# Kernel optimization log

Measured on AMD Instinct MI355X. Metric: run time of the kernel, lower is better.

The kernel has to match this reference:

```python
import jax, jax.numpy as jnp
import numpy as np
import math

B, S, E, H = 2, 2048, 1024, 16
HD = E // H          # head_dim = 64
HX = 64              # helix_dim
P = HX // 2          # helix pairs = 32

def setup_inputs() -> dict:
    key = jax.random.key(0)
    ks = jax.random.split(key, 12)
    sc = 0.02
    return {
        "x":    jax.random.normal(ks[0], (B, S, E), dtype=jnp.float32),
        "Wq":   jax.random.normal(ks[1], (E, E), dtype=jnp.float32) * sc,
        "bq":   jnp.zeros((E,), dtype=jnp.float32),
        "Wk":   jax.random.normal(ks[2], (E, E), dtype=jnp.float32) * sc,
        "bk":   jnp.zeros((E,), dtype=jnp.float32),
        "Wv":   jax.random.normal(ks[3], (E, E), dtype=jnp.float32) * sc,
        "bv":   jnp.zeros((E,), dtype=jnp.float32),
        "Wo":   jax.random.normal(ks[4], (E, E), dtype=jnp.float32) * sc,
        "bo":   jnp.zeros((E,), dtype=jnp.float32),
        "Whel": jax.random.normal(ks[5], (H, HX, HD), dtype=jnp.float32) * sc,
        "bhel": jnp.zeros((H, HX), dtype=jnp.float32),
    }

def _l2norm(x, eps=1e-12):
    # torch F.normalize(p=2, dim=-1): x / max(||x||, eps)
    n = jnp.sqrt(jnp.sum(x * x, axis=-1, keepdims=True))
    return x / jnp.maximum(n, eps)

def _scramble(t):
    # faithful to torch: (B,S,2) -> transpose(1,2) -> reshape(B,S,2),
    # vectorized over (H,P): t is (B,H,P,S,2)
    b, h, p, s, _ = t.shape
    return jnp.swapaxes(t, -1, -2).reshape(b, h, p, s, 2)

def reference(x, Wq, bq, Wk, bk, Wv, bv, Wo, bo, Whel, bhel):
    b, s, e = x.shape
    h, hx, hd = Whel.shape
    p = hx // 2
    q = x @ Wq.T + bq
    k = x @ Wk.T + bk
    v = x @ Wv.T + bv
    qh = q.reshape(b, s, h, hd)
    kh = k.reshape(b, s, h, hd)
    # per-head helical projections: (B,S,H,HX)
    q_hel = jnp.einsum('bshd,hed->bshe', qh, Whel) + bhel
    k_hel = jnp.einsum('bshd,hed->bshe', kh, Whel) + bhel
    # split into 2D coords, normalize each pair: (B,H,P,S,2)
    qn = _l2norm(q_hel.reshape(b, s, h, p, 2)).transpose(0, 2, 3, 1, 4)
    kn = _l2norm(k_hel.reshape(b, s, h, p, 2)).transpose(0, 2, 3, 1, 4)
    qn = _scramble(qn)
    kn = _scramble(kn)
    # helical similarity averaged over pairs: (B,H,S,S)
    helical = jnp.einsum('bhpsc,bhptc->bhst', qn, kn) / p
    # standard scaled dot-product scores
    dot = jnp.einsum('bshd,bthd->bhst', qh, kh) / math.sqrt(hd)
    alpha = 0.5
    attn = jax.nn.softmax(alpha * dot + (1.0 - alpha) * helical, axis=-1)
    vh = v.reshape(b, s, h, hd)
    out = jnp.einsum('bhst,bthd->bshd', attn, vh).reshape(b, s, e)
    return out @ Wo.T + bo
```

## Files before the change

kernel.cpp:

```cpp
#include <hip/hip_runtime.h>
#include <hip/hip_bf16.h>


typedef unsigned short u16;
typedef unsigned int u32;
typedef __attribute__((ext_vector_type(8))) __bf16 bf16x8;
typedef __attribute__((ext_vector_type(4))) float f32x4;
typedef __attribute__((ext_vector_type(16))) float f32x16;

union BFrag { u32 u[4]; bf16x8 b; };

__device__ __forceinline__ u16 f2b(float f) {
  u32 u = __float_as_uint(f);
  u32 r = (u + 0x7fffu + ((u >> 16) & 1u)) >> 16;
  return (u16)r;
}
__device__ __forceinline__ float b2f(u16 h) {
  return __uint_as_float(((u32)h) << 16);
}

__device__ __forceinline__ f32x4 mfma16(bf16x8 a, bf16x8 b, f32x4 c) {
  return __builtin_amdgcn_mfma_f32_16x16x32_bf16(a, b, c, 0, 0, 0);
}
__device__ __forceinline__ f32x16 mfma32(bf16x8 a, bf16x8 b, f32x16 c) {
  return __builtin_amdgcn_mfma_f32_32x32x16_bf16(a, b, c, 0, 0, 0);
}

__device__ __forceinline__ void gld16(void* lds, const void* g) {
  __builtin_amdgcn_global_load_lds(
      (const __attribute__((address_space(1))) unsigned int*)g,
      (__attribute__((address_space(3))) unsigned int*)lds, 16, 0, 0);
}

#define LOG2E 1.4426950408889634f

__global__ __launch_bounds__(256) void cast_kernel(
    const float* __restrict__ x,  const float* __restrict__ wq,
    const float* __restrict__ wk, const float* __restrict__ wv,
    const float* __restrict__ wo, const float* __restrict__ whel,
    u16* __restrict__ xb, u16* __restrict__ wb, u16* __restrict__ wob,
    u16* __restrict__ whb) {
  long long q = (long long)blockIdx.x * 256 + threadIdx.x;
  const float* s; u16* d; long long base;
  if (q < 1048576)      { s = x;    d = xb;            base = 0; }
  else if (q < 1310720) { s = wq;   d = wb;            base = 1048576; }
  else if (q < 1572864) { s = wk;   d = wb + 1048576;  base = 1310720; }
  else if (q < 1835008) { s = wv;   d = wb + 2097152;  base = 1572864; }
  else if (q < 2097152) { s = wo;   d = wob;           base = 1835008; }
  else                  { s = whel; d = whb;           base = 2097152; }
  long long e = (q - base) * 4;
  float4 v = *(const float4*)(s + e);
  ushort4 o;
  o.x = f2b(v.x); o.y = f2b(v.y); o.z = f2b(v.z); o.w = f2b(v.w);
  *(ushort4*)(d + e) = o;
}

__global__ __launch_bounds__(256, 3) void qkv_gemm(
    const u16* __restrict__ xb, const u16* __restrict__ wb,
    const float* __restrict__ bq, const float* __restrict__ bk,
    const float* __restrict__ bv,
    u16* __restrict__ Qcat, u16* __restrict__ Kcat, u16* __restrict__ vt) {
  __shared__ u16 Al[2][128][32];
  __shared__ u16 Bl[2][128][32];
  __shared__ u16 T[64][136];
  const int nt = blockIdx.x, mt = blockIdx.y;
  const int which = nt >> 3;
  const int n0 = (nt & 7) << 7;
  const int m0 = mt << 7;
  const int tid = threadIdx.x;
  const int wave = tid >> 6, lane = tid & 63;
  const int g = lane >> 4, c15 = lane & 15;
  const int wm = wave & 1, wn = wave >> 1;
  const u16* Wp = wb + (long long)which * (1024 * 1024) + n0 * 1024;
  const u16* Ap = xb + m0 * 1024;
  const int srow = (wave * 64 + lane) >> 2;
  const int scol = (lane & 3) << 3;

  f32x4 acc[4][4];
#pragma unroll
  for (int i = 0; i < 4; i++)
#pragma unroll
    for (int j = 0; j < 4; j++) acc[i][j] = f32x4{0.f, 0.f, 0.f, 0.f};

  gld16(&Al[0][srow][scol],      Ap + srow * 1024 + scol);
  gld16(&Al[0][64 + srow][scol], Ap + (64 + srow) * 1024 + scol);
  gld16(&Bl[0][srow][scol],      Wp + srow * 1024 + scol);
  gld16(&Bl[0][64 + srow][scol], Wp + (64 + srow) * 1024 + scol);

  for (int k0 = 0; k0 < 1024; k0 += 32) {
    const int c = (k0 >> 5) & 1;
    __syncthreads();
    if (k0 + 32 < 1024) {
      const int kn = k0 + 32;
      gld16(&Al[c ^ 1][srow][scol],      Ap + srow * 1024 + kn + scol);
      gld16(&Al[c ^ 1][64 + srow][scol], Ap + (64 + srow) * 1024 + kn + scol);
      gld16(&Bl[c ^ 1][srow][scol],      Wp + srow * 1024 + kn + scol);
      gld16(&Bl[c ^ 1][64 + srow][scol], Wp + (64 + srow) * 1024 + kn + scol);
    }
    bf16x8 a[4], b[4];
#pragma unroll
    for (int i = 0; i < 4; i++)
      a[i] = *(const bf16x8*)&Al[c][wm * 64 + i * 16 + c15][g * 8];
#pragma unroll
    for (int j = 0; j < 4; j++)
      b[j] = *(const bf16x8*)&Bl[c][wn * 64 + j * 16 + c15][g * 8];
#pragma unroll
    for (int i = 0; i < 4; i++)
#pragma unroll
      for (int j = 0; j < 4; j++) acc[i][j] = mfma16(a[i], b[j], acc[i][j]);
  }

  if (which == 2) {
#pragma unroll
    for (int half = 0; half < 2; ++half) {
      __syncthreads();
      if (wn == half) {
#pragma unroll
        for (int i = 0; i < 4; i++)
#pragma unroll
          for (int j = 0; j < 4; j++)
#pragma unroll
            for (int r = 0; r < 4; r++) {
              int nloc = j * 16 + c15;
              int mloc = wm * 64 + i * 16 + g * 4 + r;
              float v = acc[i][j][r] + bv[n0 + half * 64 + nloc];
              T[nloc][mloc] = f2b(v);
            }
      }
      __syncthreads();
#pragma unroll
      for (int it = 0; it < 4; ++it) {
        int idx = it * 256 + tid;
        int row = idx >> 4;
        int cm = (idx & 15) * 8;
        int col = n0 + half * 64 + row;
        int hh = col >> 6, dd = col & 63;
        int m = m0 + cm;
        int bb2 = m >> 11, s = m & 2047;
        *(uint4*)&vt[(((bb2 * 16 + hh) * 64) + dd) * 2048 + s] =
            *(const uint4*)&T[row][cm];
      }
    }
    return;
  }

  const float* bias = (which == 0) ? bq : bk;
#pragma unroll
  for (int i = 0; i < 4; i++)
#pragma unroll
    for (int j = 0; j < 4; j++)
#pragma unroll
      for (int r = 0; r < 4; r++) {
        int row = m0 + wm * 64 + i * 16 + g * 4 + r;
        int col = n0 + wn * 64 + j * 16 + c15;
        float v = acc[i][j][r] + bias[col];
        int bb = row >> 11, s = row & 2047;
        int hh = col >> 6, d = col & 63;
        if (which == 0) {
          Qcat[(((bb * 16 + hh) * 2048) + s) * 128 + d] =
              f2b(v * (0.0625f * LOG2E));
        } else {
          Kcat[(((bb * 16 + hh) * 2048) + s) * 128 + d] = f2b(v);
        }
      }
}

__global__ __launch_bounds__(256, 2) void helical_kernel(
    u16* __restrict__ Qcat, u16* __restrict__ Kcat,
    const u16* __restrict__ whb, const float* __restrict__ bhel) {
  __shared__ u16 A[2][2][64][32];
  __shared__ u16 Wl[2][64][32];
  const int sb = blockIdx.x, bh = blockIdx.y;
  const int h = bh & 15;
  const int s0 = sb << 6;
  const int tid = threadIdx.x;
  const int wave = tid >> 6, lane = tid & 63;
  const int g = lane >> 4, c15 = lane & 15;
  u16* Qb = Qcat + (long long)bh * (2048 * 128);
  u16* Kb = Kcat + (long long)bh * (2048 * 128);

#pragma unroll
  for (int it = 0; it < 2; ++it) {
    int cidx = it * 256 + tid;
    int e = cidx >> 3, ds = (cidx & 7) << 3;
    uint4 vv = *(const uint4*)(whb + h * 4096 + e * 64 + ds);
    *(uint4*)&Wl[ds >> 5][e][ds & 31] = vv;
  }
#pragma unroll
  for (int it = 0; it < 4; ++it) {
    int cidx = it * 256 + tid;
    int which = cidx >> 9;
    int r = (cidx >> 3) & 63;
    int ds = (cidx & 7) << 3;
    const u16* src = (which ? Kb : Qb) + (s0 + r) * 128 + ds;
    uint4 vv = *(const uint4*)src;
    if (which == 0) {
      u16 tmp[8];
      *(uint4*)tmp = vv;
#pragma unroll
      for (int q = 0; q < 8; ++q)
        tmp[q] = f2b(b2f(tmp[q]) * (16.0f / LOG2E));
      vv = *(uint4*)tmp;
    }
    *(uint4*)&A[which][ds >> 5][r][ds & 31] = vv;
  }
  __syncthreads();

  const int which = wave >> 1, hf = wave & 1;
  f32x4 acc[2][4];
#pragma unroll
  for (int i = 0; i < 2; i++)
#pragma unroll
    for (int j = 0; j < 4; j++) acc[i][j] = f32x4{0.f, 0.f, 0.f, 0.f};
#pragma unroll
  for (int kq = 0; kq < 2; ++kq) {
    bf16x8 a0 = *(const bf16x8*)&A[which][kq][hf * 32 + c15][g * 8];
    bf16x8 a1 = *(const bf16x8*)&A[which][kq][hf * 32 + 16 + c15][g * 8];
#pragma unroll
    for (int j = 0; j < 4; ++j) {
      bf16x8 bb = *(const bf16x8*)&Wl[kq][j * 16 + c15][g * 8];
      acc[0][j] = mfma16(a0, bb, acc[0][j]);
      acc[1][j] = mfma16(a1, bb, acc[1][j]);
    }
  }
  u16* Dst = which ? Kb : Qb;
  const float oscale = which ? 0.125f : (0.125f * LOG2E);
#pragma unroll
  for (int i = 0; i < 2; ++i)
#pragma unroll
    for (int j = 0; j < 4; ++j)
#pragma unroll
      for (int r = 0; r < 4; ++r) {
        int s_loc = hf * 32 + i * 16 + g * 4 + r;
        int e = j * 16 + c15;
        float v = acc[i][j][r] + bhel[h * 64 + e];
        float pp = __shfl_xor(v, 1);
        float nn = sqrtf(v * v + pp * pp);
        float o = v / fmaxf(nn, 1e-12f) * oscale;
        int s = s0 + s_loc;
        int u = s >> 1, c2 = s & 1;
        int row_out = ((e & 1) ? 1024 : 0) + u;
        int col_out = 64 + (e & ~1) + c2;
        Dst[row_out * 128 + col_out] = f2b(o);
      }
}

__global__ __launch_bounds__(256, 2) void attn_kernel(
    const u16* __restrict__ Qcat, const u16* __restrict__ Kcat,
    const u16* __restrict__ vt, u16* __restrict__ AO) {
  __shared__ u16 Kl[2][64][128];
  __shared__ u16 Vl[2][64][64];
  __shared__ float denl[2][128];
  const int qt = blockIdx.x, bh = blockIdx.y;
  const int bb = bh >> 4, h = bh & 15;
  const int q0 = qt << 7;
  const int tid = threadIdx.x;
  const int w = tid >> 6, lane = tid & 63;
  const int wq2 = w & 1, wt = w >> 1;
  const int l31 = lane & 31, l5 = lane >> 5;
  const u16* Qb = Qcat + (long long)bh * (2048 * 128);
  const u16* Kb = Kcat + (long long)bh * (2048 * 128);
  const u16* Vb = vt + (long long)bh * (64 * 2048);

  bf16x8 qf[2][8];
#pragma unroll
  for (int qh = 0; qh < 2; ++qh) {
    const u16* qrow = Qb + (q0 + 64 * wq2 + 32 * qh + l31) * 128 + l5 * 8;
#pragma unroll
    for (int ks = 0; ks < 8; ++ks)
      qf[qh][ks] = *(const bf16x8*)(qrow + ks * 16);
  }

  int krowR[4], ksrcR[4];
#pragma unroll
  for (int rk = 0; rk < 4; ++rk) {
    int id = rk * 256 + tid;
    int row = id >> 4, kp = id & 15;
    krowR[rk] = row;
    ksrcR[rk] = (kp & 8) | ((kp & 7) ^ (row & 7));
  }
  int vdR[2], vsrcR[2];
#pragma unroll
  for (int rv = 0; rv < 2; ++rv) {
    int id = rv * 256 + tid;
    int d = id >> 3;
    vdR[rv] = d;
    vsrcR[rv] = (id & 7) ^ (d & 7);
  }

#pragma unroll
  for (int rk = 0; rk < 4; ++rk)
    gld16(((u16*)Kl[0]) + (rk * 256 + tid) * 8,
          Kb + krowR[rk] * 128 + ksrcR[rk] * 8);
#pragma unroll
  for (int rv = 0; rv < 2; ++rv)
    gld16(((u16*)Vl[0]) + (rv * 256 + tid) * 8,
          Vb + vdR[rv] * 2048 + vsrcR[rv] * 8);

  f32x16 accO[2][2];
#pragma unroll
  for (int a = 0; a < 2; ++a)
#pragma unroll
    for (int b = 0; b < 2; ++b)
#pragma unroll
      for (int i = 0; i < 16; ++i) accO[a][b][i] = 0.f;
  float den[2] = {0.f, 0.f};

  const int krow = 32 * wt + l31;
  const int kr7 = krow & 7;

  for (int t = 0; t < 32; ++t) {
    const int cur = t & 1;
    __syncthreads();
    if (t + 1 < 32) {
      const int t1 = (t + 1) << 6;
      u16* Kd = (u16*)Kl[cur ^ 1];
      u16* Vd = (u16*)Vl[cur ^ 1];
#pragma unroll
      for (int rk = 0; rk < 4; ++rk)
        gld16(Kd + (rk * 256 + tid) * 8,
              Kb + (t1 + krowR[rk]) * 128 + ksrcR[rk] * 8);
#pragma unroll
      for (int rv = 0; rv < 2; ++rv)
        gld16(Vd + (rv * 256 + tid) * 8,
              Vb + vdR[rv] * 2048 + t1 + vsrcR[rv] * 8);
    }

    f32x16 accS0, accS1;
#pragma unroll
    for (int i = 0; i < 16; ++i) { accS0[i] = 0.f; accS1[i] = 0.f; }
#pragma unroll
    for (int ks = 0; ks < 8; ++ks) {
      int lc = 2 * ks + l5;
      int p = (lc & 8) | ((lc & 7) ^ kr7);
      bf16x8 ak = *(const bf16x8*)&Kl[cur][krow][p * 8];
      accS0 = mfma32(ak, qf[0][ks], accS0);
      accS1 = mfma32(ak, qf[1][ks], accS1);
    }

    BFrag PA[2][2];
#pragma unroll
    for (int qh = 0; qh < 2; ++qh) {
      const f32x16& s = qh ? accS1 : accS0;
      u32 D0[2], D1[2], D2[2], D3[2];
#pragma unroll
      for (int rr = 0; rr < 4; ++rr) {
        float p0 = __builtin_amdgcn_exp2f(s[4 * rr + 0]);
        float p1 = __builtin_amdgcn_exp2f(s[4 * rr + 1]);
        float p2 = __builtin_amdgcn_exp2f(s[4 * rr + 2]);
        float p3 = __builtin_amdgcn_exp2f(s[4 * rr + 3]);
        den[qh] += (p0 + p1) + (p2 + p3);
        u32 lo =
            (__float_as_uint(p0) >> 16) | (__float_as_uint(p1) & 0xffff0000u);
        u32 hi =
            (__float_as_uint(p2) >> 16) | (__float_as_uint(p3) & 0xffff0000u);
        if (rr == 0) { D0[0] = lo; D0[1] = hi; }
        else if (rr == 1) { D1[0] = lo; D1[1] = hi; }
        else if (rr == 2) { D2[0] = lo; D2[1] = hi; }
        else { D3[0] = lo; D3[1] = hi; }
      }
      u32 e00 = __shfl_xor((int)D0[0], 32), e01 = __shfl_xor((int)D0[1], 32);
      u32 e10 = __shfl_xor((int)D1[0], 32), e11 = __shfl_xor((int)D1[1], 32);
      u32 e20 = __shfl_xor((int)D2[0], 32), e21 = __shfl_xor((int)D2[1], 32);
      u32 e30 = __shfl_xor((int)D3[0], 32), e31 = __shfl_xor((int)D3[1], 32);
      PA[qh][0].u[0] = l5 ? e10 : D0[0];
      PA[qh][0].u[1] = l5 ? e11 : D0[1];
      PA[qh][0].u[2] = l5 ? D1[0] : e00;
      PA[qh][0].u[3] = l5 ? D1[1] : e01;
      PA[qh][1].u[0] = l5 ? e30 : D2[0];
      PA[qh][1].u[1] = l5 ? e31 : D2[1];
      PA[qh][1].u[2] = l5 ? D3[0] : e20;
      PA[qh][1].u[3] = l5 ? D3[1] : e21;
    }

#pragma unroll
    for (int dq = 0; dq < 2; ++dq) {
      int d = 32 * dq + l31;
      int d7 = d & 7;
#pragma unroll
      for (int ks = 0; ks < 2; ++ks) {
        int lc = 4 * wt + 2 * ks + l5;
        bf16x8 bvf = *(const bf16x8*)&Vl[cur][d][((lc ^ d7) & 7) * 8];
        accO[0][dq] = mfma32(PA[0][ks].b, bvf, accO[0][dq]);
        accO[1][dq] = mfma32(PA[1][ks].b, bvf, accO[1][dq]);
      }
    }
  }

  den[0] += __shfl_xor(den[0], 32);
  den[1] += __shfl_xor(den[1], 32);
  if (l5 == 0) {
    denl[wt][64 * wq2 + l31] = den[0];
    denl[wt][64 * wq2 + 32 + l31] = den[1];
  }
  __syncthreads();

  float* S = (float*)Kl;
  if (wt == 1) {
#pragma unroll
    for (int qh = 0; qh < 2; ++qh)
#pragma unroll
      for (int dq = 0; dq < 2; ++dq)
#pragma unroll
        for (int r = 0; r < 16; ++r) {
          int qr = (r & 3) + 8 * (r >> 2) + 4 * l5;
          S[(64 * wq2 + 32 * qh + qr) * 64 + 32 * dq + l31] = accO[qh][dq][r];
        }
  }
  __syncthreads();
  if (wt == 0) {
#pragma unroll
    for (int qh = 0; qh < 2; ++qh)
#pragma unroll
      for (int r = 0; r < 16; ++r) {
        int qr = (r & 3) + 8 * (r >> 2) + 4 * l5;
        int ql = 64 * wq2 + 32 * qh + qr;
        float inv = 1.0f / (denl[0][ql] + denl[1][ql]);
        long long base = ((long long)(bb * 2048 + q0 + ql) * 1024) + h * 64;
#pragma unroll
        for (int dq = 0; dq < 2; ++dq) {
          float o = (accO[qh][dq][r] + S[ql * 64 + 32 * dq + l31]) * inv;
          AO[base + 32 * dq + l31] = f2b(o);
        }
      }
  }
}

__global__ __launch_bounds__(256, 2) void out_gemm(
    const u16* __restrict__ AO, const u16* __restrict__ wob,
    const float* __restrict__ bo, float* __restrict__ out) {
  __shared__ u16 Al[2][128][32];
  __shared__ u16 Bl[2][128][32];
  const int n0 = blockIdx.x << 7;
  const int m0 = blockIdx.y << 7;
  const int tid = threadIdx.x;
  const int wave = tid >> 6, lane = tid & 63;
  const int g = lane >> 4, c15 = lane & 15;
  const int wm = wave & 1, wn = wave >> 1;
  const u16* Wp = wob + n0 * 1024;
  const u16* Ap = AO + m0 * 1024;
  const int srow = (wave * 64 + lane) >> 2;
  const int scol = (lane & 3) << 3;

  f32x4 acc[4][4];
#pragma unroll
  for (int i = 0; i < 4; i++)
#pragma unroll
    for (int j = 0; j < 4; j++) acc[i][j] = f32x4{0.f, 0.f, 0.f, 0.f};

  gld16(&Al[0][srow][scol],      Ap + srow * 1024 + scol);
  gld16(&Al[0][64 + srow][scol], Ap + (64 + srow) * 1024 + scol);
  gld16(&Bl[0][srow][scol],      Wp + srow * 1024 + scol);
  gld16(&Bl[0][64 + srow][scol], Wp + (64 + srow) * 1024 + scol);

  for (int k0 = 0; k0 < 1024; k0 += 32) {
    const int c = (k0 >> 5) & 1;
    __syncthreads();
    if (k0 + 32 < 1024) {
      const int kn = k0 + 32;
      gld16(&Al[c ^ 1][srow][scol],      Ap + srow * 1024 + kn + scol);
      gld16(&Al[c ^ 1][64 + srow][scol], Ap + (64 + srow) * 1024 + kn + scol);
      gld16(&Bl[c ^ 1][srow][scol],      Wp + srow * 1024 + kn + scol);
      gld16(&Bl[c ^ 1][64 + srow][scol], Wp + (64 + srow) * 1024 + kn + scol);
    }
    bf16x8 a[4], b[4];
#pragma unroll
    for (int i = 0; i < 4; i++)
      a[i] = *(const bf16x8*)&Al[c][wm * 64 + i * 16 + c15][g * 8];
#pragma unroll
    for (int j = 0; j < 4; j++)
      b[j] = *(const bf16x8*)&Bl[c][wn * 64 + j * 16 + c15][g * 8];
#pragma unroll
    for (int i = 0; i < 4; i++)
#pragma unroll
      for (int j = 0; j < 4; j++) acc[i][j] = mfma16(a[i], b[j], acc[i][j]);
  }
#pragma unroll
  for (int i = 0; i < 4; i++)
#pragma unroll
    for (int j = 0; j < 4; j++)
#pragma unroll
      for (int r = 0; r < 4; r++) {
        int row = m0 + wm * 64 + i * 16 + g * 4 + r;
        int col = n0 + wn * 64 + j * 16 + c15;
        out[row * 1024 + col] = acc[i][j][r] + bo[col];
      }
}

extern "C" void kernel_launch(void* const* d_in, const int* in_sizes, int n_in,
                              void* d_out, int out_size, void* d_ws,
                              size_t ws_size, hipStream_t stream) {
  const float* x    = (const float*)d_in[0];
  const float* Wq   = (const float*)d_in[1];
  const float* bq   = (const float*)d_in[2];
  const float* Wk   = (const float*)d_in[3];
  const float* bk   = (const float*)d_in[4];
  const float* Wv   = (const float*)d_in[5];
  const float* bv   = (const float*)d_in[6];
  const float* Wo   = (const float*)d_in[7];
  const float* bo   = (const float*)d_in[8];
  const float* Whel = (const float*)d_in[9];
  const float* bhel = (const float*)d_in[10];
  float* out = (float*)d_out;

  char* ws = (char*)d_ws;
  u16* xb   = (u16*)(ws + 0);
  u16* wb   = (u16*)(ws + 8388608);
  u16* wob  = (u16*)(ws + 14680064);
  u16* whb  = (u16*)(ws + 16777216);
  u16* Qcat = (u16*)(ws + 16908288);
  u16* Kcat = (u16*)(ws + 33685504);
  u16* vt   = (u16*)(ws + 50462720);
  u16* AO   = (u16*)(ws + 58851328);

  cast_kernel<<<dim3(8256), dim3(256), 0, stream>>>(x, Wq, Wk, Wv, Wo, Whel,
                                                    xb, wb, wob, whb);
  qkv_gemm<<<dim3(24, 32), dim3(256), 0, stream>>>(xb, wb, bq, bk, bv, Qcat,
                                                   Kcat, vt);
  helical_kernel<<<dim3(32, 32), dim3(256), 0, stream>>>(Qcat, Kcat, whb,
                                                         bhel);
  attn_kernel<<<dim3(16, 32), dim3(256), 0, stream>>>(Qcat, Kcat, vt, AO);
  out_gemm<<<dim3(8, 32), dim3(256), 0, stream>>>(AO, wob, bo, out);
}
```

Measured before the change: 232.1 us.

## Load attention K/V fragments directly into registers, drop LDS and cross-wave reduction

The attention kernel now runs 2 waves per block, each owning 64 query rows and iterating over all keys. K and V fragments are loaded from global memory straight into registers with a two-stage software double buffer, replacing the LDS staging and per-iteration barriers. The end-of-kernel LDS reduction across key-split waves is replaced by an in-register normalization using a shuffled denominator and a fast reciprocal. This removes synchronization and LDS traffic, but lowers occupancy and loses K/V sharing across waves, adding more global/L2 reads and high register pressure.

Result: slower. 271.6 us (+17.0%).

```diff
diff --git a/kernel.cpp b/kernel.cpp
--- a/kernel.cpp
+++ b/kernel.cpp
@@ -245,19 +245,15 @@
       }
 }
 
-__global__ __launch_bounds__(256, 2) void attn_kernel(
+__global__ __launch_bounds__(128, 1) void attn_kernel(
     const u16* __restrict__ Qcat, const u16* __restrict__ Kcat,
     const u16* __restrict__ vt, u16* __restrict__ AO) {
-  __shared__ u16 Kl[2][64][128];
-  __shared__ u16 Vl[2][64][64];
-  __shared__ float denl[2][128];
-  const int qt = blockIdx.x, bh = blockIdx.y;
+  const int qg = blockIdx.x, bh = blockIdx.y;
   const int bb = bh >> 4, h = bh & 15;
-  const int q0 = qt << 7;
   const int tid = threadIdx.x;
   const int w = tid >> 6, lane = tid & 63;
-  const int wq2 = w & 1, wt = w >> 1;
   const int l31 = lane & 31, l5 = lane >> 5;
+  const int qw = qg * 128 + w * 64;
   const u16* Qb = Qcat + (long long)bh * (2048 * 128);
   const u16* Kb = Kcat + (long long)bh * (2048 * 128);
   const u16* Vb = vt + (long long)bh * (64 * 2048);
@@ -265,37 +261,14 @@
   bf16x8 qf[2][8];
 #pragma unroll
   for (int qh = 0; qh < 2; ++qh) {
-    const u16* qrow = Qb + (q0 + 64 * wq2 + 32 * qh + l31) * 128 + l5 * 8;
+    const u16* qrow = Qb + (qw + 32 * qh + l31) * 128 + l5 * 8;
 #pragma unroll
     for (int ks = 0; ks < 8; ++ks)
       qf[qh][ks] = *(const bf16x8*)(qrow + ks * 16);
   }
 
-  int krowR[4], ksrcR[4];
-#pragma unroll
-  for (int rk = 0; rk < 4; ++rk) {
-    int id = rk * 256 + tid;
-    int row = id >> 4, kp = id & 15;
-    krowR[rk] = row;
-    ksrcR[rk] = (kp & 8) | ((kp & 7) ^ (row & 7));
-  }
-  int vdR[2], vsrcR[2];
-#pragma unroll
-  for (int rv = 0; rv < 2; ++rv) {
-    int id = rv * 256 + tid;
-    int d = id >> 3;
-    vdR[rv] = d;
-    vsrcR[rv] = (id & 7) ^ (d & 7);
-  }
-
-#pragma unroll
-  for (int rk = 0; rk < 4; ++rk)
-    gld16(((u16*)Kl[0]) + (rk * 256 + tid) * 8,
-          Kb + krowR[rk] * 128 + ksrcR[rk] * 8);
-#pragma unroll
-  for (int rv = 0; rv < 2; ++rv)
-    gld16(((u16*)Vl[0]) + (rv * 256 + tid) * 8,
-          Vb + vdR[rv] * 2048 + vsrcR[rv] * 8);
+  const u16* kbase = Kb + l31 * 128 + l5 * 8;
+  const u16* vbase = Vb + l31 * 2048 + l5 * 8;
 
   f32x16 accO[2][2];
 #pragma unroll
@@ -306,124 +279,107 @@
       for (int i = 0; i < 16; ++i) accO[a][b][i] = 0.f;
   float den[2] = {0.f, 0.f};
 
-  const int krow = 32 * wt + l31;
-  const int kr7 = krow & 7;
-
-  for (int t = 0; t < 32; ++t) {
-    const int cur = t & 1;
-    __syncthreads();
-    if (t + 1 < 32) {
-      const int t1 = (t + 1) << 6;
-      u16* Kd = (u16*)Kl[cur ^ 1];
-      u16* Vd = (u16*)Vl[cur ^ 1];
-#pragma unroll
-      for (int rk = 0; rk < 4; ++rk)
-        gld16(Kd + (rk * 256 + tid) * 8,
-              Kb + (t1 + krowR[rk]) * 128 + ksrcR[rk] * 8);
-#pragma unroll
-      for (int rv = 0; rv < 2; ++rv)
-        gld16(Vd + (rv * 256 + tid) * 8,
-              Vb + vdR[rv] * 2048 + t1 + vsrcR[rv] * 8);
-    }
-
-    f32x16 accS0, accS1;
-#pragma unroll
-    for (int i = 0; i < 16; ++i) { accS0[i] = 0.f; accS1[i] = 0.f; }
-#pragma unroll
-    for (int ks = 0; ks < 8; ++ks) {
-      int lc = 2 * ks + l5;
-      int p = (lc & 8) | ((lc & 7) ^ kr7);
-      bf16x8 ak = *(const bf16x8*)&Kl[cur][krow][p * 8];
-      accS0 = mfma32(ak, qf[0][ks], accS0);
-      accS1 = mfma32(ak, qf[1][ks], accS1);
-    }
-
-    BFrag PA[2][2];
-#pragma unroll
-    for (int qh = 0; qh < 2; ++qh) {
-      const f32x16& s = qh ? accS1 : accS0;
-      u32 D0[2], D1[2], D2[2], D3[2];
-#pragma unroll
-      for (int rr = 0; rr < 4; ++rr) {
-        float p0 = __builtin_amdgcn_exp2f(s[4 * rr + 0]);
-        float p1 = __builtin_amdgcn_exp2f(s[4 * rr + 1]);
-        float p2 = __builtin_amdgcn_exp2f(s[4 * rr + 2]);
-        float p3 = __builtin_amdgcn_exp2f(s[4 * rr + 3]);
-        den[qh] += (p0 + p1) + (p2 + p3);
-        u32 lo =
-            (__float_as_uint(p0) >> 16) | (__float_as_uint(p1) & 0xffff0000u);
-        u32 hi =
-            (__float_as_uint(p2) >> 16) | (__float_as_uint(p3) & 0xffff0000u);
-        if (rr == 0) { D0[0] = lo; D0[1] = hi; }
-        else if (rr == 1) { D1[0] = lo; D1[1] = hi; }
-        else if (rr == 2) { D2[0] = lo; D2[1] = hi; }
-        else { D3[0] = lo; D3[1] = hi; }
-      }
-      u32 e00 = __shfl_xor((int)D0[0], 32), e01 = __shfl_xor((int)D0[1], 32);
-      u32 e10 = __shfl_xor((int)D1[0], 32), e11 = __shfl_xor((int)D1[1], 32);
-      u32 e20 = __shfl_xor((int)D2[0], 32), e21 = __shfl_xor((int)D2[1], 32);
-      u32 e30 = __shfl_xor((int)D3[0], 32), e31 = __shfl_xor((int)D3[1], 32);
-      PA[qh][0].u[0] = l5 ? e10 : D0[0];
-      PA[qh][0].u[1] = l5 ? e11 : D0[1];
-      PA[qh][0].u[2] = l5 ? D1[0] : e00;
-      PA[qh][0].u[3] = l5 ? D1[1] : e01;
-      PA[qh][1].u[0] = l5 ? e30 : D2[0];
-      PA[qh][1].u[1] = l5 ? e31 : D2[1];
-      PA[qh][1].u[2] = l5 ? D3[0] : e20;
-      PA[qh][1].u[3] = l5 ? D3[1] : e21;
-    }
-
-#pragma unroll
-    for (int dq = 0; dq < 2; ++dq) {
-      int d = 32 * dq + l31;
-      int d7 = d & 7;
-#pragma unroll
-      for (int ks = 0; ks < 2; ++ks) {
-        int lc = 4 * wt + 2 * ks + l5;
-        bf16x8 bvf = *(const bf16x8*)&Vl[cur][d][((lc ^ d7) & 7) * 8];
-        accO[0][dq] = mfma32(PA[0][ks].b, bvf, accO[0][dq]);
-        accO[1][dq] = mfma32(PA[1][ks].b, bvf, accO[1][dq]);
-      }
-    }
+  auto ldt = [&](int t, bf16x8 (&kf)[2][8], bf16x8 (&vf)[2][4]) {
+    const u16* kt = kbase + t * 8192;
+#pragma unroll
+    for (int sl = 0; sl < 2; ++sl)
+#pragma unroll
+      for (int ks = 0; ks < 8; ++ks)
+        kf[sl][ks] = *(const bf16x8*)(kt + sl * 4096 + ks * 16);
+    const u16* vtp = vbase + t * 64;
+#pragma unroll
+    for (int dq = 0; dq < 2; ++dq)
+#pragma unroll
+      for (int c = 0; c < 4; ++c)
+        vf[dq][c] = *(const bf16x8*)(vtp + dq * 65536 + c * 16);
+  };
+
+  auto step = [&](bf16x8 (&kf)[2][8], bf16x8 (&vf)[2][4]) {
+    f32x16 aS[2][2];
+#pragma unroll
+    for (int sl = 0; sl < 2; ++sl)
+#pragma unroll
+      for (int qh = 0; qh < 2; ++qh)
+#pragma unroll
+        for (int i = 0; i < 16; ++i) aS[sl][qh][i] = 0.f;
+#pragma unroll
+    for (int sl = 0; sl < 2; ++sl)
+#pragma unroll
+      for (int ks = 0; ks < 8; ++ks) {
+        bf16x8 ak = kf[sl][ks];
+        aS[sl][0] = mfma32(ak, qf[0][ks], aS[sl][0]);
+        aS[sl][1] = mfma32(ak, qf[1][ks], aS[sl][1]);
+      }
+#pragma unroll
+    for (int sl = 0; sl < 2; ++sl) {
+      BFrag PA[2][2];
+#pragma unroll
+      for (int qh = 0; qh < 2; ++qh) {
+        u32 D0[2], D1[2], D2[2], D3[2];
+#pragma unroll
+        for (int rr = 0; rr < 4; ++rr) {
+          float p0 = __builtin_amdgcn_exp2f(aS[sl][qh][4 * rr + 0]);
+          float p1 = __builtin_amdgcn_exp2f(aS[sl][qh][4 * rr + 1]);
+          float p2 = __builtin_amdgcn_exp2f(aS[sl][qh][4 * rr + 2]);
+          float p3 = __builtin_amdgcn_exp2f(aS[sl][qh][4 * rr + 3]);
+          den[qh] += (p0 + p1) + (p2 + p3);
+          u32 lo = (__float_as_uint(p0) >> 16) |
+                   (__float_as_uint(p1) & 0xffff0000u);
+          u32 hi = (__float_as_uint(p2) >> 16) |
+                   (__float_as_uint(p3) & 0xffff0000u);
+          if (rr == 0) { D0[0] = lo; D0[1] = hi; }
+          else if (rr == 1) { D1[0] = lo; D1[1] = hi; }
+          else if (rr == 2) { D2[0] = lo; D2[1] = hi; }
+          else { D3[0] = lo; D3[1] = hi; }
+        }
+        u32 e00 = __shfl_xor((int)D0[0], 32), e01 = __shfl_xor((int)D0[1], 32);
+        u32 e10 = __shfl_xor((int)D1[0], 32), e11 = __shfl_xor((int)D1[1], 32);
+        u32 e20 = __shfl_xor((int)D2[0], 32), e21 = __shfl_xor((int)D2[1], 32);
+        u32 e30 = __shfl_xor((int)D3[0], 32), e31 = __shfl_xor((int)D3[1], 32);
+        PA[qh][0].u[0] = l5 ? e10 : D0[0];
+        PA[qh][0].u[1] = l5 ? e11 : D0[1];
+        PA[qh][0].u[2] = l5 ? D1[0] : e00;
+        PA[qh][0].u[3] = l5 ? D1[1] : e01;
+        PA[qh][1].u[0] = l5 ? e30 : D2[0];
+        PA[qh][1].u[1] = l5 ? e31 : D2[1];
+        PA[qh][1].u[2] = l5 ? D3[0] : e20;
+        PA[qh][1].u[3] = l5 ? D3[1] : e21;
+      }
+#pragma unroll
+      for (int dq = 0; dq < 2; ++dq) {
+        bf16x8 bv0 = vf[dq][sl * 2 + 0];
+        bf16x8 bv1 = vf[dq][sl * 2 + 1];
+        accO[0][dq] = mfma32(PA[0][0].b, bv0, accO[0][dq]);
+        accO[0][dq] = mfma32(PA[0][1].b, bv1, accO[0][dq]);
+        accO[1][dq] = mfma32(PA[1][0].b, bv0, accO[1][dq]);
+        accO[1][dq] = mfma32(PA[1][1].b, bv1, accO[1][dq]);
+      }
+    }
+  };
+
+  bf16x8 kfA[2][8], vfA[2][4], kfB[2][8], vfB[2][4];
+  ldt(0, kfA, vfA);
+  for (int t = 0; t < 32; t += 2) {
+    ldt(t + 1, kfB, vfB);
+    step(kfA, vfA);
+    if (t + 2 < 32) ldt(t + 2, kfA, vfA);
+    step(kfB, vfB);
   }
 
   den[0] += __shfl_xor(den[0], 32);
   den[1] += __shfl_xor(den[1], 32);
-  if (l5 == 0) {
-    denl[wt][64 * wq2 + l31] = den[0];
-    denl[wt][64 * wq2 + 32 + l31] = den[1];
-  }
-  __syncthreads();
-
-  float* S = (float*)Kl;
-  if (wt == 1) {
-#pragma unroll
-    for (int qh = 0; qh < 2; ++qh)
-#pragma unroll
-      for (int dq = 0; dq < 2; ++dq)
-#pragma unroll
-        for (int r = 0; r < 16; ++r) {
-          int qr = (r & 3) + 8 * (r >> 2) + 4 * l5;
-          S[(64 * wq2 + 32 * qh + qr) * 64 + 32 * dq + l31] = accO[qh][dq][r];
-        }
-  }
-  __syncthreads();
-  if (wt == 0) {
-#pragma unroll
-    for (int qh = 0; qh < 2; ++qh)
-#pragma unroll
-      for (int r = 0; r < 16; ++r) {
-        int qr = (r & 3) + 8 * (r >> 2) + 4 * l5;
-        int ql = 64 * wq2 + 32 * qh + qr;
-        float inv = 1.0f / (denl[0][ql] + denl[1][ql]);
-        long long base = ((long long)(bb * 2048 + q0 + ql) * 1024) + h * 64;
-#pragma unroll
-        for (int dq = 0; dq < 2; ++dq) {
-          float o = (accO[qh][dq][r] + S[ql * 64 + 32 * dq + l31]) * inv;
-          AO[base + 32 * dq + l31] = f2b(o);
-        }
-      }
-  }
+#pragma unroll
+  for (int qh = 0; qh < 2; ++qh)
+#pragma unroll
+    for (int r = 0; r < 16; ++r) {
+      int rowl = (r & 3) + 8 * (r >> 2) + 4 * l5;
+      float dr = __shfl(den[qh], rowl);
+      float inv = __builtin_amdgcn_rcpf(dr);
+      int q = qw + 32 * qh + rowl;
+      long long base = ((long long)(bb * 2048 + q) * 1024) + h * 64;
+      AO[base + l31]      = f2b(accO[qh][0][r] * inv);
+      AO[base + 32 + l31] = f2b(accO[qh][1][r] * inv);
+    }
 }
 
 __global__ __launch_bounds__(256, 2) void out_gemm(
@@ -519,6 +475,6 @@
                                                    Kcat, vt);
   helical_kernel<<<dim3(32, 32), dim3(256), 0, stream>>>(Qcat, Kcat, whb,
                                                          bhel);
-  attn_kernel<<<dim3(16, 32), dim3(256), 0, stream>>>(Qcat, Kcat, vt, AO);
+  attn_kernel<<<dim3(16, 32), dim3(128), 0, stream>>>(Qcat, Kcat, vt, AO);
   out_gemm<<<dim3(8, 32), dim3(256), 0, stream>>>(AO, wob, bo, out);
 }
```
